# Kernel tuning notes

Measured on AMD Instinct MI355X. Metric: run time of the kernel, lower is better.

## Reference

```python
import jax, jax.numpy as jnp
import numpy as np

N_NODES = 50000
N_EDGES = 800000
IN_F = 128
OUT_F = 128
N_REL = 40
N_BASES = 30


def setup_inputs() -> dict:
    key = jax.random.key(0)
    k = jax.random.split(key, 8)
    x = jax.random.normal(k[0], (N_NODES, IN_F), dtype=jnp.float32)
    edge_index = jax.random.randint(k[1], (2, N_EDGES), 0, N_NODES, dtype=jnp.int64)
    edge_type = jax.random.randint(k[2], (N_EDGES,), 0, N_REL, dtype=jnp.int64)
    # Xavier-uniform-ish parameter init
    def xavier(kk, shape):
        fan_in, fan_out = shape[-2], shape[-1]
        a = float(np.sqrt(6.0 / (fan_in + fan_out)))
        return jax.random.uniform(kk, shape, jnp.float32, -a, a)
    weight = xavier(k[3], (N_BASES, IN_F, OUT_F))
    coeff = xavier(k[4], (N_REL, N_BASES))
    self_weight = xavier(k[5], (IN_F, OUT_F))
    bias = jnp.zeros((OUT_F,), dtype=jnp.float32)
    return {
        "x": x,
        "edge_index": edge_index,
        "edge_type": edge_type,
        "num_nodes": N_NODES,
        "weight": weight,
        "coeff": coeff,
        "self_weight": self_weight,
        "bias": bias,
    }


def reference(x, edge_index, edge_type, num_nodes, weight, coeff, self_weight, bias):
    # Basis decomposition: W_r = sum_b coeff[r,b] * V_b -> [R, in, out]
    rel_weight = jnp.einsum("rb,bio->rio", coeff, weight)
    # Since msg = x[src] @ W[r] == (x @ W[r])[src], transform all nodes for
    # all relations once, then gather per edge. h_all: [R, N, out]
    h_all = jnp.einsum("ni,rio->rno", x, rel_weight)
    src = edge_index[0]
    tgt = edge_index[1]
    msg = h_all[edge_type, src]  # [E, out]
    out = jax.ops.segment_sum(msg, tgt, num_segments=num_nodes)  # scatter-add
    # in-degree normalization, clamped at 1
    deg = jax.ops.segment_sum(jnp.ones_like(tgt, dtype=x.dtype), tgt,
                              num_segments=num_nodes)
    deg = jnp.maximum(deg, 1.0)
    out = out / deg[:, None]
    out = out + x @ self_weight  # self loop
    out = out + bias
    return out
```

## Files before the change

kernel.cpp:

```cpp
#include <hip/hip_runtime.h>

#define IN_F 128
#define OUT_F 128
#define MSG_GRID 2048

typedef unsigned int uint;
typedef unsigned short ushort;
typedef __attribute__((ext_vector_type(8))) short bf16x8;
typedef __attribute__((ext_vector_type(4))) float f32x4;
typedef __attribute__((ext_vector_type(4))) float f32x4e;
typedef __attribute__((ext_vector_type(2))) float f32x2e;
typedef __attribute__((ext_vector_type(4))) int i32x4;
typedef __attribute__((ext_vector_type(2))) uint u32x2e;

typedef __attribute__((address_space(1))) void gvoid;
typedef __attribute__((address_space(3))) void svoid;

__device__ __forceinline__ void gl_lds16(const void* g, void* l) {
  __builtin_amdgcn_global_load_lds((const gvoid*)g, (svoid*)l, 16, 0, 0);
}

__device__ inline ushort f2bf(float f) {
  uint u = __float_as_uint(f);
  uint r = (u + 0x7FFFu + ((u >> 16) & 1u)) >> 16;
  return (ushort)r;
}

__global__ __launch_bounds__(256) void k_prep(
    const float* __restrict__ w, const float* __restrict__ coef,
    const float* __restrict__ selfw, ushort* __restrict__ rwT,
    const float* __restrict__ x, ushort* __restrict__ xbf, int n4,
    const int* __restrict__ etype, const int* __restrict__ tgt, int E, int R, int B,
    int* __restrict__ hist, int* __restrict__ ideg, int wblocks, int xblocks) {
  __shared__ float t[64][65];
  __shared__ int lh[64];
  int tid = threadIdx.x;
  int bid = blockIdx.x;

  if (bid < wblocks) {
    int r = bid >> 2;
    int i0 = (bid & 1) * 64;
    int o0 = ((bid >> 1) & 1) * 64;
    float4 a4[4];
    if (r < R) {
      #pragma unroll
      for (int it = 0; it < 4; ++it) a4[it] = make_float4(0.f, 0.f, 0.f, 0.f);
      for (int b = 0; b < B; ++b) {
        float cb = coef[r * B + b];
        const float4* w4 = (const float4*)w + (size_t)b * 4096;
        #pragma unroll
        for (int it = 0; it < 4; ++it) {
          int idx = it * 256 + tid;
          int i = idx >> 4, c4 = idx & 15;
          float4 v = w4[(i0 + i) * 32 + (o0 >> 2) + c4];
          a4[it].x = fmaf(cb, v.x, a4[it].x);
          a4[it].y = fmaf(cb, v.y, a4[it].y);
          a4[it].z = fmaf(cb, v.z, a4[it].z);
          a4[it].w = fmaf(cb, v.w, a4[it].w);
        }
      }
    } else {
      const float4* w4 = (const float4*)selfw;
      #pragma unroll
      for (int it = 0; it < 4; ++it) {
        int idx = it * 256 + tid;
        int i = idx >> 4, c4 = idx & 15;
        a4[it] = w4[(i0 + i) * 32 + (o0 >> 2) + c4];
      }
    }
    #pragma unroll
    for (int it = 0; it < 4; ++it) {
      int idx = it * 256 + tid;
      int i = idx >> 4, c4 = idx & 15;
      t[i][c4 * 4 + 0] = a4[it].x; t[i][c4 * 4 + 1] = a4[it].y;
      t[i][c4 * 4 + 2] = a4[it].z; t[i][c4 * 4 + 3] = a4[it].w;
    }
    __syncthreads();
    ushort* dst = rwT + (size_t)r * IN_F * OUT_F;
    #pragma unroll
    for (int it = 0; it < 4; ++it) {
      int idx = it * 256 + tid;
      int o = idx >> 4, cc = idx & 15;
      uint2 pk;
      pk.x = (uint)f2bf(t[cc * 4 + 0][o]) | ((uint)f2bf(t[cc * 4 + 1][o]) << 16);
      pk.y = (uint)f2bf(t[cc * 4 + 2][o]) | ((uint)f2bf(t[cc * 4 + 3][o]) << 16);
      *(uint2*)(dst + (o0 + o) * IN_F + i0 + cc * 4) = pk;
    }
    return;
  }
  bid -= wblocks;
  if (bid < xblocks) {
    int i = bid * 256 + tid;
    if (i < n4) {
      f32x4e v = __builtin_nontemporal_load((const f32x4e*)x + i);
      uint2 pk;
      pk.x = (uint)f2bf(v.x) | ((uint)f2bf(v.y) << 16);
      pk.y = (uint)f2bf(v.z) | ((uint)f2bf(v.w) << 16);
      ((uint2*)xbf)[i] = pk;
    }
    return;
  }
  bid -= xblocks;
  if (tid < R) lh[tid] = 0;
  __syncthreads();
  int e = bid * 256 + tid;
  if (e < E) {
    atomicAdd(&lh[etype[e]], 1);
    atomicAdd(&ideg[tgt[e]], 1);
  }
  __syncthreads();
  if (tid < R && lh[tid]) atomicAdd(&hist[tid], lh[tid]);
}

__global__ __launch_bounds__(1024) void k_scans(
    const int* __restrict__ hist, int* __restrict__ offs, int* __restrict__ toffs,
    int R, const int* __restrict__ ideg, int* __restrict__ row_off, int N) {
  __shared__ int part[1024];
  int tid = threadIdx.x;
  if (tid == 0) {
    int s = 0, tt = 0;
    for (int r = 0; r < R; ++r) {
      offs[r] = s; toffs[r] = tt;
      s += hist[r];
      tt += (hist[r] + 63) >> 6;
    }
    offs[R] = s; toffs[R] = tt;
  }
  int chunk = (((N + 1023) >> 10) + 3) & ~3;
  int lo = min(tid * chunk, N), hi = min(lo + chunk, N);
  int s = 0;
  int i = lo;
  for (; i + 4 <= hi; i += 4) {
    i32x4 v = *(const i32x4*)(ideg + i);
    s += v.x + v.y + v.z + v.w;
  }
  for (; i < hi; ++i) s += ideg[i];
  part[tid] = s;
  __syncthreads();
  for (int d = 1; d < 1024; d <<= 1) {
    int v = (tid >= d) ? part[tid - d] : 0;
    __syncthreads();
    part[tid] += v;
    __syncthreads();
  }
  int pre = (tid > 0) ? part[tid - 1] : 0;
  i = lo;
  for (; i + 4 <= hi; i += 4) {
    i32x4 v = *(const i32x4*)(ideg + i);
    i32x4 o;
    o.x = pre; o.y = pre + v.x; o.z = o.y + v.y; o.w = o.z + v.z;
    pre = o.w + v.w;
    *(i32x4*)(row_off + i) = o;
  }
  for (; i < hi; ++i) { row_off[i] = pre; pre += ideg[i]; }
  if (tid == 1023) row_off[N] = part[1023];
}

__global__ void k_scatter2(const int* __restrict__ etype, const int* __restrict__ src,
                           const int* __restrict__ tgt, int E, int R,
                           const int* __restrict__ offs, const int* __restrict__ row_off,
                           int* __restrict__ cur_r, int* __restrict__ cur_t,
                           int* __restrict__ perm, int* __restrict__ wpos) {
  __shared__ int lh[64], lbase[64], lcur[64];
  int tid = threadIdx.x;
  if (tid < R) { lh[tid] = 0; lcur[tid] = 0; }
  __syncthreads();
  int e = blockIdx.x * blockDim.x + tid;
  int t = -1;
  if (e < E) { t = etype[e]; atomicAdd(&lh[t], 1); }
  __syncthreads();
  if (tid < R) lbase[tid] = lh[tid] ? atomicAdd(&cur_r[tid], lh[tid]) : 0;
  __syncthreads();
  if (e < E) {
    int loc = atomicAdd(&lcur[t], 1);
    int slot = offs[t] + lbase[t] + loc;
    perm[slot] = src[e];
    int tg = tgt[e];
    int pos = row_off[tg] + atomicAdd(&cur_t[tg], 1);
    wpos[slot] = pos;
  }
}

__global__ __launch_bounds__(256) void k_msg(
    const ushort* __restrict__ xbf, const int* __restrict__ perm,
    const int* __restrict__ wpos, const int* __restrict__ offs,
    const int* __restrict__ toffs, const ushort* __restrict__ rwT,
    ushort* __restrict__ msg, int R) {
  __shared__ ushort xs[2][64 * IN_F];
  __shared__ int soff[48], stoff[48];
  int tid = threadIdx.x, wv = tid >> 6, l = tid & 63, g = l >> 4, ln = l & 15;
  int wc = wv * 32;
  int trow = tid >> 4, ts4 = tid & 15;

  if (tid <= R) { soff[tid] = offs[tid]; stoff[tid] = toffs[tid]; }
  __syncthreads();
  int ntiles = stoff[R];
  int chunkT = (ntiles + MSG_GRID - 1) / MSG_GRID;
  int t0 = blockIdx.x * chunkT;
  int tend = min(t0 + chunkT, ntiles);
  if (t0 >= tend) return;

  bf16x8 bfr[2][4];
#define LOADW(rr)                                                             \
  {                                                                           \
    const ushort* _wp = rwT + (size_t)(rr) * IN_F * OUT_F;                    \
    _Pragma("unroll")                                                         \
    for (int _n = 0; _n < 2; ++_n)                                            \
      _Pragma("unroll")                                                       \
      for (int _kk = 0; _kk < 4; ++_kk)                                       \
        bfr[_n][_kk] = *(const bf16x8*)(_wp + (wc + _n * 16 + ln) * IN_F +    \
                                        _kk * 32 + g * 8);                    \
  }

  int r0 = 0;
  while (t0 >= stoff[r0 + 1]) ++r0;

  bf16x8 xreg[4];
  int srcrow[4], wq[4];

  {
    int eb = soff[r0] + (t0 - stoff[r0]) * 64;
    int cnt = min(64, soff[r0 + 1] - eb);
    #pragma unroll
    for (int i = 0; i < 4; ++i) {
      int row = trow + 16 * i;
      int sr = perm[eb + min(row, cnt - 1)];
      xreg[i] = *(const bf16x8*)(xbf + (size_t)sr * IN_F + ts4 * 8);
    }
    #pragma unroll
    for (int i = 0; i < 4; ++i) {
      int row = trow + 16 * i;
      *(bf16x8*)((char*)xs[0] + row * 256 + ((ts4 * 16) ^ ((row & 7) << 4))) = xreg[i];
    }
    #pragma unroll
    for (int q = 0; q < 4; ++q) wq[q] = wpos[eb + min(q * 16 + ln, cnt - 1)];
  }
  if (t0 + 1 < tend) {
    int r1 = r0; while (t0 + 1 >= stoff[r1 + 1]) ++r1;
    int eb = soff[r1] + (t0 + 1 - stoff[r1]) * 64;
    int cnt = min(64, soff[r1 + 1] - eb);
    #pragma unroll
    for (int i = 0; i < 4; ++i) {
      int row = trow + 16 * i;
      int sr = perm[eb + min(row, cnt - 1)];
      xreg[i] = *(const bf16x8*)(xbf + (size_t)sr * IN_F + ts4 * 8);
    }
  }
  if (t0 + 2 < tend) {
    int r2 = r0; while (t0 + 2 >= stoff[r2 + 1]) ++r2;
    int eb = soff[r2] + (t0 + 2 - stoff[r2]) * 64;
    int cnt = min(64, soff[r2 + 1] - eb);
    #pragma unroll
    for (int i = 0; i < 4; ++i)
      srcrow[i] = perm[eb + min(trow + 16 * i, cnt - 1)];
  }
  LOADW(r0)
  int r_loaded = r0;
  int rcw = r0, rw1 = r0, rw3 = r0;
  int cur = 0;

  for (int t = t0; t < tend; ++t) {
    asm volatile("s_waitcnt lgkmcnt(0)" ::: "memory");
    __builtin_amdgcn_s_barrier();
    __builtin_amdgcn_sched_barrier(0);

    while (t >= stoff[rcw + 1]) ++rcw;
    int eb_t = soff[rcw] + (t - stoff[rcw]) * 64;
    int cnt_t = min(64, soff[rcw + 1] - eb_t);
    if (rcw != r_loaded) { LOADW(rcw) r_loaded = rcw; }

    const char* xb = (const char*)xs[cur];
    f32x4 acc[2][4] = {};
    #pragma unroll
    for (int kk = 0; kk < 4; ++kk) {
      bf16x8 a[4];
      #pragma unroll
      for (int q = 0; q < 4; ++q) {
        int row = q * 16 + ln;
        int kb = kk * 64 + g * 16;
        a[q] = *(const bf16x8*)(xb + row * 256 + (kb ^ ((row & 7) << 4)));
      }
      #pragma unroll
      for (int n = 0; n < 2; ++n)
        #pragma unroll
        for (int q = 0; q < 4; ++q)
          acc[n][q] = __builtin_amdgcn_mfma_f32_16x16x32_bf16(bfr[n][kk], a[q],
                                                              acc[n][q], 0, 0, 0);
    }

    #pragma unroll
    for (int q = 0; q < 4; ++q) {
      int rr = q * 16 + ln;
      if (rr < cnt_t) {
        ushort* mp = msg + (size_t)wq[q] * OUT_F + wc + g * 4;
        uint2 p0, p1;
        p0.x = (uint)f2bf(acc[0][q][0]) | ((uint)f2bf(acc[0][q][1]) << 16);
        p0.y = (uint)f2bf(acc[0][q][2]) | ((uint)f2bf(acc[0][q][3]) << 16);
        p1.x = (uint)f2bf(acc[1][q][0]) | ((uint)f2bf(acc[1][q][1]) << 16);
        p1.y = (uint)f2bf(acc[1][q][2]) | ((uint)f2bf(acc[1][q][3]) << 16);
        *(uint2*)mp = p0;
        *(uint2*)(mp + 16) = p1;
      }
    }

    if (t + 1 < tend) {
      char* xw = (char*)xs[cur ^ 1];
      #pragma unroll
      for (int i = 0; i < 4; ++i) {
        int row = trow + 16 * i;
        *(bf16x8*)(xw + row * 256 + ((ts4 * 16) ^ ((row & 7) << 4))) = xreg[i];
      }
    }

    if (t + 2 < tend) {
      #pragma unroll
      for (int i = 0; i < 4; ++i)
        xreg[i] = *(const bf16x8*)(xbf + (size_t)srcrow[i] * IN_F + ts4 * 8);
    }
    if (t + 3 < tend) {
      while (t + 3 >= stoff[rw3 + 1]) ++rw3;
      int eb = soff[rw3] + (t + 3 - stoff[rw3]) * 64;
      int cnt = min(64, soff[rw3 + 1] - eb);
      #pragma unroll
      for (int i = 0; i < 4; ++i)
        srcrow[i] = perm[eb + min(trow + 16 * i, cnt - 1)];
    }
    if (t + 1 < tend) {
      while (t + 1 >= stoff[rw1 + 1]) ++rw1;
      int eb = soff[rw1] + (t + 1 - stoff[rw1]) * 64;
      int cnt = min(64, soff[rw1 + 1] - eb);
      #pragma unroll
      for (int q = 0; q < 4; ++q) wq[q] = wpos[eb + min(q * 16 + ln, cnt - 1)];
    }
    cur ^= 1;
  }
#undef LOADW
}

__global__ __launch_bounds__(256) void k_out(
    const ushort* __restrict__ xbf, const ushort* __restrict__ swT,
    const float* __restrict__ bias, const ushort* __restrict__ msg,
    const int* __restrict__ row_off, float* __restrict__ out, int N) {
  __shared__ float smem[64 * 128];
  int tid = threadIdx.x;
  int base = blockIdx.x * 64;
  int wv = tid >> 6, l = tid & 63;
  char* xb = (char*)smem;

  #pragma unroll
  for (int i = 0; i < 4; ++i) {
    int idx = i * 256 + tid;
    int row = idx >> 4, s4 = idx & 15;
    int c = s4 ^ (row & 7);
    int n = base + row;
    char* lb = xb + i * 4096 + wv * 1024;
    if (n < N)
      gl_lds16(xbf + (size_t)n * IN_F + c * 8, lb);
  }

  int g = l >> 4, ln = l & 15, wc = wv * 32;
  bf16x8 bfr[2][4];
  #pragma unroll
  for (int n = 0; n < 2; ++n)
    #pragma unroll
    for (int kk = 0; kk < 4; ++kk)
      bfr[n][kk] = *(const bf16x8*)(swT + (wc + n * 16 + ln) * IN_F + kk * 32 + g * 8);

  __syncthreads();

  f32x4 acc[4][2] = {};
  #pragma unroll
  for (int kk = 0; kk < 4; ++kk) {
    bf16x8 a[4];
    #pragma unroll
    for (int m = 0; m < 4; ++m) {
      int row = m * 16 + ln;
      int kb = kk * 64 + g * 16;
      a[m] = *(const bf16x8*)(xb + row * 256 + (kb ^ ((row & 7) << 4)));
    }
    #pragma unroll
    for (int m = 0; m < 4; ++m)
      #pragma unroll
      for (int n = 0; n < 2; ++n)
        acc[m][n] = __builtin_amdgcn_mfma_f32_16x16x32_bf16(a[m], bfr[n][kk],
                                                            acc[m][n], 0, 0, 0);
  }

  __syncthreads();
  #pragma unroll
  for (int m = 0; m < 4; ++m)
    #pragma unroll
    for (int n = 0; n < 2; ++n)
      #pragma unroll
      for (int j = 0; j < 4; ++j)
        smem[(m * 16 + g * 4 + j) * 128 + wc + n * 16 + ln] = acc[m][n][j];
  __syncthreads();

  int half = l >> 5, cl = l & 31;
  f32x4e b4 = ((const f32x4e*)bias)[cl];
  for (int q = 0; q < 16; ++q) {
    int n = base + wv * 16 + q;
    if (n >= N) break;
    int lo = row_off[n], hi = row_off[n + 1];
    int len = hi - lo;
    const ushort* mrow = msg + (size_t)(lo + half) * OUT_F + cl * 4;
    float fa0 = 0.f, fa1 = 0.f, fa2 = 0.f, fa3 = 0.f;
#define ACC8(v)                                                  \
    { fa0 += __uint_as_float((v).x << 16);                       \
      fa1 += __uint_as_float((v).x & 0xFFFF0000u);               \
      fa2 += __uint_as_float((v).y << 16);                       \
      fa3 += __uint_as_float((v).y & 0xFFFF0000u); }
    int p = 0;
    for (; p + 8 <= len; p += 8) {
      u32x2e v0 = *(const u32x2e*)(mrow + (size_t)p * OUT_F);
      u32x2e v1 = *(const u32x2e*)(mrow + (size_t)(p + 2) * OUT_F);
      u32x2e v2 = *(const u32x2e*)(mrow + (size_t)(p + 4) * OUT_F);
      u32x2e v3 = *(const u32x2e*)(mrow + (size_t)(p + 6) * OUT_F);
      ACC8(v0) ACC8(v1) ACC8(v2) ACC8(v3)
    }
    for (; p + 2 <= len; p += 2) {
      u32x2e v = *(const u32x2e*)(mrow + (size_t)p * OUT_F);
      ACC8(v)
    }
    if (p < len && half == 0) {
      u32x2e v = *(const u32x2e*)(mrow + (size_t)p * OUT_F);
      ACC8(v)
    }
#undef ACC8
    fa0 += __shfl_xor(fa0, 32);
    fa1 += __shfl_xor(fa1, 32);
    fa2 += __shfl_xor(fa2, 32);
    fa3 += __shfl_xor(fa3, 32);
    if (half == 0) {
      float inv = 1.f / (float)max(len, 1);
      int rloc = wv * 16 + q;
      f32x4e s4 = *(const f32x4e*)(&smem[rloc * 128 + cl * 4]);
      f32x4e o = {fa0 * inv + s4.x + b4.x, fa1 * inv + s4.y + b4.y,
                  fa2 * inv + s4.z + b4.z, fa3 * inv + s4.w + b4.w};
      __builtin_nontemporal_store(o, (f32x4e*)(out + (size_t)n * OUT_F + cl * 4));
    }
  }
}

extern "C" void kernel_launch(void* const* d_in, const int* in_sizes, int n_in,
                              void* d_out, int out_size, void* d_ws, size_t ws_size,
                              hipStream_t stream) {
  const float* x      = (const float*)d_in[0];
  const int*   ei     = (const int*)d_in[1];
  const int*   etype  = (const int*)d_in[2];
  const float* weight = (const float*)d_in[4];
  const float* coeff  = (const float*)d_in[5];
  const float* selfw  = (const float*)d_in[6];
  const float* bias   = (const float*)d_in[7];

  int N = in_sizes[0] / IN_F;
  int E = in_sizes[2];
  int B = in_sizes[4] / (IN_F * OUT_F);
  int R = in_sizes[5] / B;
  const int* src = ei;
  const int* tgt = ei + E;

  char* ws = (char*)d_ws;
  size_t off = 0;
  auto alloc = [&](size_t bytes) {
    char* p = ws + off;
    off += (bytes + 255) & ~(size_t)255;
    return p;
  };
  ushort* rwT     = (ushort*)alloc((size_t)(R + 1) * IN_F * OUT_F * 2);
  ushort* xbf     = (ushort*)alloc((size_t)N * IN_F * 2);
  int*    perm    = (int*)alloc((size_t)E * 4);
  int*    wpos    = (int*)alloc((size_t)E * 4);
  int*    row_off = (int*)alloc((size_t)(N + 1) * 4);
  int*    ideg    = (int*)alloc((size_t)(2 * N + 128) * 4);
  int*    cur_t   = ideg + N;
  int*    hist    = cur_t + N;
  int*    cur_r   = hist + 64;
  int*    offs    = (int*)alloc(64 * 4);
  int*    toffs   = (int*)alloc(64 * 4);
  ushort* msg     = (ushort*)alloc((size_t)E * OUT_F * 2);

  (void)hipMemsetAsync(ideg, 0, (size_t)(2 * N + 128) * 4, stream);

  int n4 = N * IN_F / 4;
  int wblocks = (R + 1) * 4;
  int xblocks = (n4 + 255) / 256;
  int hblocks = (E + 255) / 256;
  k_prep<<<wblocks + xblocks + hblocks, 256, 0, stream>>>(
      weight, coeff, selfw, rwT, x, xbf, n4, etype, tgt, E, R, B,
      hist, ideg, wblocks, xblocks);
  k_scans<<<1, 1024, 0, stream>>>(hist, offs, toffs, R, ideg, row_off, N);
  k_scatter2<<<hblocks, 256, 0, stream>>>(etype, src, tgt, E, R, offs, row_off,
                                          cur_r, cur_t, perm, wpos);
  k_msg<<<MSG_GRID, 256, 0, stream>>>(xbf, perm, wpos, offs, toffs, rwT, msg, R);
  k_out<<<(N + 63) / 64, 256, 0, stream>>>(xbf, rwT + (size_t)R * IN_F * OUT_F,
                                           bias, msg, row_off, (float*)d_out, N);
}
```

Baseline: 295.4 us.

## Bin edges by relation and source block to improve gather locality

Replaces the per-relation counting sort with a finer sort on (relation, src>>8) bins, so edges within each relation are grouped by source-node range. This is meant to improve cache locality of the x row gathers in the message kernel. The scatter kernel now does a global atomic per edge on 10240 bin counters instead of block-local aggregation, which risks more atomic contention, and the scan kernel gains a second block-wide scan. k_out also stages its row offsets in shared memory.

```diff
diff --git a/kernel.cpp b/kernel.cpp
--- a/kernel.cpp
+++ b/kernel.cpp
@@ -30,10 +30,10 @@
     const float* __restrict__ w, const float* __restrict__ coef,
     const float* __restrict__ selfw, ushort* __restrict__ rwT,
     const float* __restrict__ x, ushort* __restrict__ xbf, int n4,
-    const int* __restrict__ etype, const int* __restrict__ tgt, int E, int R, int B,
-    int* __restrict__ hist, int* __restrict__ ideg, int wblocks, int xblocks) {
+    const int* __restrict__ etype, const int* __restrict__ src,
+    const int* __restrict__ tgt, int E, int R, int B,
+    int* __restrict__ binhist, int* __restrict__ ideg, int wblocks, int xblocks) {
   __shared__ float t[64][65];
-  __shared__ int lh[64];
   int tid = threadIdx.x;
   int bid = blockIdx.x;
 
@@ -101,40 +101,25 @@
     return;
   }
   bid -= xblocks;
-  if (tid < R) lh[tid] = 0;
-  __syncthreads();
   int e = bid * 256 + tid;
   if (e < E) {
-    atomicAdd(&lh[etype[e]], 1);
+    int bin = etype[e] * 256 + (src[e] >> 8);
+    atomicAdd(&binhist[bin], 1);
     atomicAdd(&ideg[tgt[e]], 1);
   }
-  __syncthreads();
-  if (tid < R && lh[tid]) atomicAdd(&hist[tid], lh[tid]);
 }
 
 __global__ __launch_bounds__(1024) void k_scans(
-    const int* __restrict__ hist, int* __restrict__ offs, int* __restrict__ toffs,
-    int R, const int* __restrict__ ideg, int* __restrict__ row_off, int N) {
+    const int* __restrict__ binhist, int* __restrict__ binoff,
+    int* __restrict__ offs, int* __restrict__ toffs, int R, int NB,
+    const int* __restrict__ ideg, int* __restrict__ row_off, int N) {
   __shared__ int part[1024];
   int tid = threadIdx.x;
-  if (tid == 0) {
-    int s = 0, tt = 0;
-    for (int r = 0; r < R; ++r) {
-      offs[r] = s; toffs[r] = tt;
-      s += hist[r];
-      tt += (hist[r] + 63) >> 6;
-    }
-    offs[R] = s; toffs[R] = tt;
-  }
-  int chunk = (((N + 1023) >> 10) + 3) & ~3;
-  int lo = min(tid * chunk, N), hi = min(lo + chunk, N);
+
+  int bchunk = (NB + 1023) >> 10;
+  int blo = min(tid * bchunk, NB), bhi = min(blo + bchunk, NB);
   int s = 0;
-  int i = lo;
-  for (; i + 4 <= hi; i += 4) {
-    i32x4 v = *(const i32x4*)(ideg + i);
-    s += v.x + v.y + v.z + v.w;
-  }
-  for (; i < hi; ++i) s += ideg[i];
+  for (int i = blo; i < bhi; ++i) s += binhist[i];
   part[tid] = s;
   __syncthreads();
   for (int d = 1; d < 1024; d <<= 1) {
@@ -144,6 +129,39 @@
     __syncthreads();
   }
   int pre = (tid > 0) ? part[tid - 1] : 0;
+  for (int i = blo; i < bhi; ++i) { binoff[i] = pre; pre += binhist[i]; }
+  if (tid == 1023) binoff[NB] = part[1023];
+  __syncthreads();
+  if (tid == 0) {
+    for (int r = 0; r < R; ++r) offs[r] = binoff[r * 256];
+    offs[R] = binoff[NB];
+    int tt = 0;
+    for (int r = 0; r < R; ++r) {
+      toffs[r] = tt;
+      tt += (offs[r + 1] - offs[r] + 63) >> 6;
+    }
+    toffs[R] = tt;
+  }
+
+  int chunk = (((N + 1023) >> 10) + 3) & ~3;
+  int lo = min(tid * chunk, N), hi = min(lo + chunk, N);
+  int s2 = 0;
+  int i = lo;
+  for (; i + 4 <= hi; i += 4) {
+    i32x4 v = *(const i32x4*)(ideg + i);
+    s2 += v.x + v.y + v.z + v.w;
+  }
+  for (; i < hi; ++i) s2 += ideg[i];
+  __syncthreads();
+  part[tid] = s2;
+  __syncthreads();
+  for (int d = 1; d < 1024; d <<= 1) {
+    int v = (tid >= d) ? part[tid - d] : 0;
+    __syncthreads();
+    part[tid] += v;
+    __syncthreads();
+  }
+  pre = (tid > 0) ? part[tid - 1] : 0;
   i = lo;
   for (; i + 4 <= hi; i += 4) {
     i32x4 v = *(const i32x4*)(ideg + i);
@@ -157,28 +175,18 @@
 }
 
 __global__ void k_scatter2(const int* __restrict__ etype, const int* __restrict__ src,
-                           const int* __restrict__ tgt, int E, int R,
-                           const int* __restrict__ offs, const int* __restrict__ row_off,
-                           int* __restrict__ cur_r, int* __restrict__ cur_t,
+                           const int* __restrict__ tgt, int E,
+                           const int* __restrict__ binoff, const int* __restrict__ row_off,
+                           int* __restrict__ bincur, int* __restrict__ cur_t,
                            int* __restrict__ perm, int* __restrict__ wpos) {
-  __shared__ int lh[64], lbase[64], lcur[64];
-  int tid = threadIdx.x;
-  if (tid < R) { lh[tid] = 0; lcur[tid] = 0; }
-  __syncthreads();
-  int e = blockIdx.x * blockDim.x + tid;
-  int t = -1;
-  if (e < E) { t = etype[e]; atomicAdd(&lh[t], 1); }
-  __syncthreads();
-  if (tid < R) lbase[tid] = lh[tid] ? atomicAdd(&cur_r[tid], lh[tid]) : 0;
-  __syncthreads();
-  if (e < E) {
-    int loc = atomicAdd(&lcur[t], 1);
-    int slot = offs[t] + lbase[t] + loc;
-    perm[slot] = src[e];
-    int tg = tgt[e];
-    int pos = row_off[tg] + atomicAdd(&cur_t[tg], 1);
-    wpos[slot] = pos;
-  }
+  int e = blockIdx.x * blockDim.x + threadIdx.x;
+  if (e >= E) return;
+  int s = src[e];
+  int bin = etype[e] * 256 + (s >> 8);
+  int pos = binoff[bin] + atomicAdd(&bincur[bin], 1);
+  perm[pos] = s;
+  int tg = tgt[e];
+  wpos[pos] = row_off[tg] + atomicAdd(&cur_t[tg], 1);
 }
 
 __global__ __launch_bounds__(256) void k_msg(
@@ -342,6 +350,7 @@
     const float* __restrict__ bias, const ushort* __restrict__ msg,
     const int* __restrict__ row_off, float* __restrict__ out, int N) {
   __shared__ float smem[64 * 128];
+  __shared__ int rof[65];
   int tid = threadIdx.x;
   int base = blockIdx.x * 64;
   int wv = tid >> 6, l = tid & 63;
@@ -357,6 +366,7 @@
     if (n < N)
       gl_lds16(xbf + (size_t)n * IN_F + c * 8, lb);
   }
+  if (tid < 65) rof[tid] = row_off[min(base + tid, N)];
 
   int g = l >> 4, ln = l & 15, wc = wv * 32;
   bf16x8 bfr[2][4];
@@ -401,7 +411,7 @@
   for (int q = 0; q < 16; ++q) {
     int n = base + wv * 16 + q;
     if (n >= N) break;
-    int lo = row_off[n], hi = row_off[n + 1];
+    int lo = rof[wv * 16 + q], hi = rof[wv * 16 + q + 1];
     int len = hi - lo;
     const ushort* mrow = msg + (size_t)(lo + half) * OUT_F + cl * 4;
     float fa0 = 0.f, fa1 = 0.f, fa2 = 0.f, fa3 = 0.f;
@@ -459,6 +469,7 @@
   int R = in_sizes[5] / B;
   const int* src = ei;
   const int* tgt = ei + E;
+  int NB = R * 256;
 
   char* ws = (char*)d_ws;
   size_t off = 0;
@@ -472,26 +483,28 @@
   int*    perm    = (int*)alloc((size_t)E * 4);
   int*    wpos    = (int*)alloc((size_t)E * 4);
   int*    row_off = (int*)alloc((size_t)(N + 1) * 4);
-  int*    ideg    = (int*)alloc((size_t)(2 * N + 128) * 4);
+  int*    binoff  = (int*)alloc((size_t)(NB + 1) * 4);
+  int*    ideg    = (int*)alloc((size_t)(2 * N + 2 * NB) * 4);
   int*    cur_t   = ideg + N;
-  int*    hist    = cur_t + N;
-  int*    cur_r   = hist + 64;
+  int*    binhist = cur_t + N;
+  int*    bincur  = binhist + NB;
   int*    offs    = (int*)alloc(64 * 4);
   int*    toffs   = (int*)alloc(64 * 4);
   ushort* msg     = (ushort*)alloc((size_t)E * OUT_F * 2);
 
-  (void)hipMemsetAsync(ideg, 0, (size_t)(2 * N + 128) * 4, stream);
+  (void)hipMemsetAsync(ideg, 0, (size_t)(2 * N + 2 * NB) * 4, stream);
 
   int n4 = N * IN_F / 4;
   int wblocks = (R + 1) * 4;
   int xblocks = (n4 + 255) / 256;
   int hblocks = (E + 255) / 256;
   k_prep<<<wblocks + xblocks + hblocks, 256, 0, stream>>>(
-      weight, coeff, selfw, rwT, x, xbf, n4, etype, tgt, E, R, B,
-      hist, ideg, wblocks, xblocks);
-  k_scans<<<1, 1024, 0, stream>>>(hist, offs, toffs, R, ideg, row_off, N);
-  k_scatter2<<<hblocks, 256, 0, stream>>>(etype, src, tgt, E, R, offs, row_off,
-                                          cur_r, cur_t, perm, wpos);
+      weight, coeff, selfw, rwT, x, xbf, n4, etype, src, tgt, E, R, B,
+      binhist, ideg, wblocks, xblocks);
+  k_scans<<<1, 1024, 0, stream>>>(binhist, binoff, offs, toffs, R, NB,
+                                  ideg, row_off, N);
+  k_scatter2<<<hblocks, 256, 0, stream>>>(etype, src, tgt, E, binoff, row_off,
+                                          bincur, cur_t, perm, wpos);
   k_msg<<<MSG_GRID, 256, 0, stream>>>(xbf, perm, wpos, offs, toffs, rwT, msg, R);
   k_out<<<(N + 63) / 64, 256, 0, stream>>>(xbf, rwT + (size_t)R * IN_F * OUT_F,
                                            bias, msg, row_off, (float*)d_out, N);
```

New measurement: 351.2 us. +18.9%, slower.
